# Optimization experiments

Measured on AMD Instinct MI355X. Metric: run time of the kernel, lower is better.

The kernel has to match this reference:

```python
import jax, jax.numpy as jnp
import numpy as np

B, V_IN, V_OUT, C_IN, C_OUT, SPIRAL, K_NNZ = 4, 12500, 50000, 64, 32, 9, 3

def setup_inputs() -> dict:
    key = jax.random.key(0)
    k1, k2, k3, k4, k5 = jax.random.split(key, 5)
    x = jax.random.normal(k1, (B, V_IN, C_IN), dtype=jnp.float32)
    spiral_indices = jax.random.randint(k2, (V_OUT, SPIRAL), 0, V_OUT)
    up_idx = jax.random.randint(k3, (V_OUT, K_NNZ), 0, V_IN)
    up_val = jax.random.uniform(k4, (V_OUT, K_NNZ), dtype=jnp.float32)
    weight = jax.random.normal(k5, (SPIRAL * C_IN, C_OUT), dtype=jnp.float32) / np.sqrt(SPIRAL * C_IN)
    bias = jnp.zeros((C_OUT,), dtype=jnp.float32)
    return {"x": x, "spiral_indices": spiral_indices, "up_idx": up_idx,
            "up_val": up_val, "weight": weight, "bias": bias}

def reference(x, spiral_indices, up_idx, up_val, weight, bias):
    # pool_bvc: sparse up_transform @ x, 3 nnz per output vertex
    # x: [B, V_in, C]; up_idx/up_val: [V_out, K]
    up = jnp.einsum('bvkc,vk->bvc', x[:, up_idx], up_val)  # [B, V_out, C_in]
    # SpiralConv: gather spiral neighborhoods, flatten, linear
    g = up[:, spiral_indices]                               # [B, V_out, S, C_in]
    g = g.reshape(g.shape[0], g.shape[1], -1)               # [B, V_out, S*C_in]
    y = jnp.einsum('bvf,fo->bvo', g, weight) + bias         # [B, V_out, C_out]
    return jax.nn.relu(y)
```

## Files before the change

kernel.cpp:

```cpp
#include <hip/hip_runtime.h>
#include <hip/hip_bf16.h>

#define B_     4
#define V_IN   12500
#define V_OUT  50000
#define C_IN   64
#define C_OUT  32
#define SPIRAL 9
#define K_NNZ  3
#define ROWS   (B_ * V_OUT)
#define GROUPS (ROWS / 16)
#define GRID1  2048
#define KDIM   (SPIRAL * C_IN)
#define KSTEPS (KDIM / 32)
#define NTILES (ROWS / 64)
#define GRID2  1024
#define WFRAG_ELEMS (KSTEPS * 2 * 64 * 8)

typedef __attribute__((ext_vector_type(8))) short short8_t;
typedef __attribute__((ext_vector_type(4))) float floatx4;

__device__ __forceinline__ unsigned short f32_to_bf16(float f) {
    unsigned int u = __float_as_uint(f);
    unsigned int r = u + 0x7fffu + ((u >> 16) & 1u);
    return (unsigned short)(r >> 16);
}

__global__ __launch_bounds__(256) void upsample_kernel(
    const float* __restrict__ x,
    const int* __restrict__ up_idx,
    const float* __restrict__ up_val,
    const float* __restrict__ weight,
    unsigned short* __restrict__ up_bf16,
    unsigned short* __restrict__ w_frag)
{
    int tid = threadIdx.x;
    if (blockIdx.x == GRID1) {
        for (int idx = tid; idx < WFRAG_ELEMS; idx += 256) {
            int j     = idx & 7;
            int lane  = (idx >> 3) & 63;
            int ntile = (idx >> 9) & 1;
            int kstep = idx >> 10;
            int k = kstep * 32 + (lane >> 4) * 8 + j;
            int n = ntile * 16 + (lane & 15);
            w_frag[idx] = f32_to_bf16(weight[k * C_OUT + n]);
        }
        return;
    }
    int lane16 = tid & 15;
    int sub    = tid >> 4;
    for (int grp = blockIdx.x; grp < GROUPS; grp += GRID1) {
        int r = grp * 16 + sub;
        int b = r / V_OUT;
        int v = r - b * V_OUT;
        const int*   ui = up_idx + v * K_NNZ;
        const float* uv = up_val + v * K_NNZ;
        float a0 = 0.f, a1 = 0.f, a2 = 0.f, a3 = 0.f;
#pragma unroll
        for (int k = 0; k < K_NNZ; k++) {
            int u = ui[k];
            float val = uv[k];
            const float4* xp = (const float4*)(x + ((size_t)b * V_IN + u) * C_IN) + lane16;
            float4 xv = *xp;
            a0 += val * xv.x; a1 += val * xv.y; a2 += val * xv.z; a3 += val * xv.w;
        }
        ushort4 o;
        o.x = f32_to_bf16(a0); o.y = f32_to_bf16(a1);
        o.z = f32_to_bf16(a2); o.w = f32_to_bf16(a3);
        *((ushort4*)(up_bf16 + (size_t)r * C_IN) + lane16) = o;
    }
}

__global__ __launch_bounds__(256) void gemm_kernel(
    const unsigned short* __restrict__ up_bf16,
    const int* __restrict__ spiral,
    const unsigned short* __restrict__ w_frag,
    const float* __restrict__ bias,
    float* __restrict__ out)
{
    __shared__ __align__(16) unsigned short w_lds[WFRAG_ELEMS];
    int tid = threadIdx.x;
    {
        const uint4* src = (const uint4*)w_frag;
        uint4* dst = (uint4*)w_lds;
#pragma unroll
        for (int i = 0; i < WFRAG_ELEMS / 8 / 256; i++)
            dst[tid + i * 256] = src[tid + i * 256];
    }
    __syncthreads();

    int wave = tid >> 6;
    int lane = tid & 63;
    int m    = lane & 15;
    int quad = lane >> 4;

    float4 bias0 = ((const float4*)bias)[quad];
    float4 bias1 = ((const float4*)bias)[4 + quad];

    for (int tile = blockIdx.x; tile < NTILES; tile += GRID2) {
        int r = tile * 64 + wave * 16 + m;
        int b = r / V_OUT;
        int v = r - b * V_OUT;
        const int* sp = spiral + v * SPIRAL;
        size_t base = (size_t)b * V_OUT * C_IN;

        short8_t g0[SPIRAL], g1[SPIRAL];
#pragma unroll
        for (int s = 0; s < SPIRAL; s++) {
            const unsigned short* rowp = up_bf16 + base + (size_t)sp[s] * C_IN;
            g0[s] = *(const short8_t*)(rowp + quad * 8);
            g1[s] = *(const short8_t*)(rowp + 32 + quad * 8);
        }

        floatx4 acc0 = {0.f, 0.f, 0.f, 0.f};
        floatx4 acc1 = {0.f, 0.f, 0.f, 0.f};
#pragma unroll
        for (int kstep = 0; kstep < KSTEPS; kstep++) {
            short8_t gf = (kstep & 1) ? g1[kstep >> 1] : g0[kstep >> 1];
            const short8_t* wp0 = (const short8_t*)(w_lds + ((kstep * 2 + 0) * 64 + lane) * 8);
            const short8_t* wp1 = (const short8_t*)(w_lds + ((kstep * 2 + 1) * 64 + lane) * 8);
            acc0 = __builtin_amdgcn_mfma_f32_16x16x32_bf16(*wp0, gf, acc0, 0, 0, 0);
            acc1 = __builtin_amdgcn_mfma_f32_16x16x32_bf16(*wp1, gf, acc1, 0, 0, 0);
        }

        float4 o0, o1;
        o0.x = acc0[0] + bias0.x; o0.y = acc0[1] + bias0.y;
        o0.z = acc0[2] + bias0.z; o0.w = acc0[3] + bias0.w;
        o1.x = acc1[0] + bias1.x; o1.y = acc1[1] + bias1.y;
        o1.z = acc1[2] + bias1.z; o1.w = acc1[3] + bias1.w;
        o0.x = o0.x > 0.f ? o0.x : 0.f;  o0.y = o0.y > 0.f ? o0.y : 0.f;
        o0.z = o0.z > 0.f ? o0.z : 0.f;  o0.w = o0.w > 0.f ? o0.w : 0.f;
        o1.x = o1.x > 0.f ? o1.x : 0.f;  o1.y = o1.y > 0.f ? o1.y : 0.f;
        o1.z = o1.z > 0.f ? o1.z : 0.f;  o1.w = o1.w > 0.f ? o1.w : 0.f;
        float* op = out + (size_t)r * C_OUT;
        *(float4*)(op + quad * 4)      = o0;
        *(float4*)(op + 16 + quad * 4) = o1;
    }
}

extern "C" void kernel_launch(void* const* d_in, const int* in_sizes, int n_in,
                              void* d_out, int out_size, void* d_ws, size_t ws_size,
                              hipStream_t stream) {
    const float* x      = (const float*)d_in[0];
    const int*   spiral = (const int*)d_in[1];
    const int*   up_idx = (const int*)d_in[2];
    const float* up_val = (const float*)d_in[3];
    const float* weight = (const float*)d_in[4];
    const float* bias   = (const float*)d_in[5];
    float* out = (float*)d_out;

    unsigned short* up_ws  = (unsigned short*)d_ws;
    unsigned short* w_frag = up_ws + (size_t)ROWS * C_IN;

    upsample_kernel<<<GRID1 + 1, 256, 0, stream>>>(x, up_idx, up_val, weight, up_ws, w_frag);
    gemm_kernel<<<GRID2, 256, 0, stream>>>(up_ws, spiral, w_frag, bias, out);
}
```

Baseline: 140.2 us.

## Map batch slices to XCDs so gathered rows stay in per-XCD L2

Remaps block indices so that each pair of XCDs (blockIdx & 7) handles one batch element, in both the upsample and GEMM kernels. Each XCD's L2 then only sees the x and up_bf16 rows of one batch, which improves cache locality for the random gathers. Tiles are now counted per batch, so the GEMM kernel gains a bounds check for the partial last tile. This relies on the assumption that blocks are dispatched round-robin across XCDs.

```diff
diff --git a/kernel.cpp b/kernel.cpp
--- a/kernel.cpp
+++ b/kernel.cpp
@@ -9,13 +9,14 @@
 #define SPIRAL 9
 #define K_NNZ  3
 #define ROWS   (B_ * V_OUT)
-#define GROUPS (ROWS / 16)
-#define GRID1  2048
 #define KDIM   (SPIRAL * C_IN)
 #define KSTEPS (KDIM / 32)
-#define NTILES (ROWS / 64)
-#define GRID2  1024
 #define WFRAG_ELEMS (KSTEPS * 2 * 64 * 8)
+
+#define GROUPS_PER_B (V_OUT / 16)
+#define G1           2048
+#define TILES_PER_B  782
+#define G2           1024
 
 typedef __attribute__((ext_vector_type(8))) short short8_t;
 typedef __attribute__((ext_vector_type(4))) float floatx4;
@@ -35,7 +36,7 @@
     unsigned short* __restrict__ w_frag)
 {
     int tid = threadIdx.x;
-    if (blockIdx.x == GRID1) {
+    if (blockIdx.x == G1) {
         for (int idx = tid; idx < WFRAG_ELEMS; idx += 256) {
             int j     = idx & 7;
             int lane  = (idx >> 3) & 63;
@@ -47,12 +48,18 @@
         }
         return;
     }
+    int xcd = blockIdx.x & 7;
+    int b   = xcd >> 1;
+    int h   = xcd & 1;
+    int j   = blockIdx.x >> 3;
     int lane16 = tid & 15;
     int sub    = tid >> 4;
-    for (int grp = blockIdx.x; grp < GROUPS; grp += GRID1) {
-        int r = grp * 16 + sub;
-        int b = r / V_OUT;
-        int v = r - b * V_OUT;
+
+    const float* xb = x + (size_t)b * V_IN * C_IN;
+    unsigned short* upb = up_bf16 + (size_t)b * V_OUT * C_IN;
+
+    for (int gl = h + 2 * j; gl < GROUPS_PER_B; gl += 512) {
+        int v = gl * 16 + sub;
         const int*   ui = up_idx + v * K_NNZ;
         const float* uv = up_val + v * K_NNZ;
         float a0 = 0.f, a1 = 0.f, a2 = 0.f, a3 = 0.f;
@@ -60,14 +67,14 @@
         for (int k = 0; k < K_NNZ; k++) {
             int u = ui[k];
             float val = uv[k];
-            const float4* xp = (const float4*)(x + ((size_t)b * V_IN + u) * C_IN) + lane16;
+            const float4* xp = (const float4*)(xb + (size_t)u * C_IN) + lane16;
             float4 xv = *xp;
             a0 += val * xv.x; a1 += val * xv.y; a2 += val * xv.z; a3 += val * xv.w;
         }
         ushort4 o;
         o.x = f32_to_bf16(a0); o.y = f32_to_bf16(a1);
         o.z = f32_to_bf16(a2); o.w = f32_to_bf16(a3);
-        *((ushort4*)(up_bf16 + (size_t)r * C_IN) + lane16) = o;
+        *((ushort4*)(upb + (size_t)v * C_IN) + lane16) = o;
     }
 }
 
@@ -94,20 +101,27 @@
     int m    = lane & 15;
     int quad = lane >> 4;
 
+    int xcd = blockIdx.x & 7;
+    int b   = xcd >> 1;
+    int h   = xcd & 1;
+    int j   = blockIdx.x >> 3;
+
+    const unsigned short* upb = up_bf16 + (size_t)b * V_OUT * C_IN;
+    float* outb = out + (size_t)b * V_OUT * C_OUT;
+
     float4 bias0 = ((const float4*)bias)[quad];
     float4 bias1 = ((const float4*)bias)[4 + quad];
 
-    for (int tile = blockIdx.x; tile < NTILES; tile += GRID2) {
-        int r = tile * 64 + wave * 16 + m;
-        int b = r / V_OUT;
-        int v = r - b * V_OUT;
+    for (int tl = h + 2 * j; tl < TILES_PER_B; tl += 256) {
+        int vr = tl * 64 + wave * 16 + m;
+        int valid = vr < V_OUT;
+        int v = valid ? vr : 0;
         const int* sp = spiral + v * SPIRAL;
-        size_t base = (size_t)b * V_OUT * C_IN;
 
         short8_t g0[SPIRAL], g1[SPIRAL];
 #pragma unroll
         for (int s = 0; s < SPIRAL; s++) {
-            const unsigned short* rowp = up_bf16 + base + (size_t)sp[s] * C_IN;
+            const unsigned short* rowp = upb + (size_t)sp[s] * C_IN;
             g0[s] = *(const short8_t*)(rowp + quad * 8);
             g1[s] = *(const short8_t*)(rowp + 32 + quad * 8);
         }
@@ -123,18 +137,20 @@
             acc1 = __builtin_amdgcn_mfma_f32_16x16x32_bf16(*wp1, gf, acc1, 0, 0, 0);
         }
 
-        float4 o0, o1;
-        o0.x = acc0[0] + bias0.x; o0.y = acc0[1] + bias0.y;
-        o0.z = acc0[2] + bias0.z; o0.w = acc0[3] + bias0.w;
-        o1.x = acc1[0] + bias1.x; o1.y = acc1[1] + bias1.y;
-        o1.z = acc1[2] + bias1.z; o1.w = acc1[3] + bias1.w;
-        o0.x = o0.x > 0.f ? o0.x : 0.f;  o0.y = o0.y > 0.f ? o0.y : 0.f;
-        o0.z = o0.z > 0.f ? o0.z : 0.f;  o0.w = o0.w > 0.f ? o0.w : 0.f;
-        o1.x = o1.x > 0.f ? o1.x : 0.f;  o1.y = o1.y > 0.f ? o1.y : 0.f;
-        o1.z = o1.z > 0.f ? o1.z : 0.f;  o1.w = o1.w > 0.f ? o1.w : 0.f;
-        float* op = out + (size_t)r * C_OUT;
-        *(float4*)(op + quad * 4)      = o0;
-        *(float4*)(op + 16 + quad * 4) = o1;
+        if (valid) {
+            float4 o0, o1;
+            o0.x = acc0[0] + bias0.x; o0.y = acc0[1] + bias0.y;
+            o0.z = acc0[2] + bias0.z; o0.w = acc0[3] + bias0.w;
+            o1.x = acc1[0] + bias1.x; o1.y = acc1[1] + bias1.y;
+            o1.z = acc1[2] + bias1.z; o1.w = acc1[3] + bias1.w;
+            o0.x = o0.x > 0.f ? o0.x : 0.f;  o0.y = o0.y > 0.f ? o0.y : 0.f;
+            o0.z = o0.z > 0.f ? o0.z : 0.f;  o0.w = o0.w > 0.f ? o0.w : 0.f;
+            o1.x = o1.x > 0.f ? o1.x : 0.f;  o1.y = o1.y > 0.f ? o1.y : 0.f;
+            o1.z = o1.z > 0.f ? o1.z : 0.f;  o1.w = o1.w > 0.f ? o1.w : 0.f;
+            float* op = outb + (size_t)vr * C_OUT;
+            *(float4*)(op + quad * 4)      = o0;
+            *(float4*)(op + 16 + quad * 4) = o1;
+        }
     }
 }
 
@@ -152,6 +168,6 @@
     unsigned short* up_ws  = (unsigned short*)d_ws;
     unsigned short* w_frag = up_ws + (size_t)ROWS * C_IN;
 
-    upsample_kernel<<<GRID1 + 1, 256, 0, stream>>>(x, up_idx, up_val, weight, up_ws, w_frag);
-    gemm_kernel<<<GRID2, 256, 0, stream>>>(up_ws, spiral, w_frag, bias, out);
+    upsample_kernel<<<G1 + 1, 256, 0, stream>>>(x, up_idx, up_val, weight, up_ws, w_frag);
+    gemm_kernel<<<G2, 256, 0, stream>>>(up_ws, spiral, w_frag, bias, out);
 }
```

Result: faster. 130.9 us (-6.6%).
